# Optimization experiments

Hardware: AMD Instinct MI355X
Metric: run time of the kernel (lower is better)

## Reference

```python
import jax, jax.numpy as jnp
import numpy as np

N_SEG = 65536          # number of output segments
TOTAL = 2097152        # total input rows (avg 32 per segment)
D = 128                # feature dim


def setup_inputs() -> dict:
    key = jax.random.key(0)
    kx, kp = jax.random.split(key)
    x = jax.random.normal(kx, (TOTAL, D), dtype=jnp.float32)
    # CSR indptr: sorted random interior boundaries, endpoints pinned to 0 and TOTAL
    inner = jnp.sort(jax.random.randint(kp, (N_SEG - 1,), 0, TOTAL, dtype=jnp.int64))
    indptr = jnp.concatenate([
        jnp.zeros((1,), dtype=jnp.int64),
        inner,
        jnp.full((1,), TOTAL, dtype=jnp.int64),
    ])  # [N_SEG + 1]
    return {"x": x, "indptr": indptr}


def _indptr_to_segment_ids(indptr, total):
    # Marker-and-cumsum: handles empty segments (duplicate indptr values) via .add
    marks = jnp.zeros((total,), dtype=jnp.int32)
    marks = marks.at[indptr[1:-1]].add(1)
    return jnp.cumsum(marks)  # [total] segment id per row


def reference(x, indptr):
    # segment_csr(x, indptr, reduce='sum'): out[i] = sum of x[indptr[i]:indptr[i+1]]
    seg_ids = _indptr_to_segment_ids(indptr, x.shape[0])
    return jax.ops.segment_sum(x, seg_ids, num_segments=N_SEG)  # [N_SEG, D]
```

## Files before the change

### kernel.cpp

```cpp
#include <hip/hip_runtime.h>


#define NSEG  65536
#define TOTAL 2097152
#define RPW   128
#define UNR   8

typedef float f32x2 __attribute__((ext_vector_type(2)));
typedef float f32x4 __attribute__((ext_vector_type(4)));

__global__ __launch_bounds__(256) void zero_out_kernel(f32x4* __restrict__ out4)
{
    const size_t i = (size_t)blockIdx.x * 256 + threadIdx.x;
    f32x4 z = {0.f, 0.f, 0.f, 0.f};
    __builtin_nontemporal_store(z, out4 + i);
}

__global__ __launch_bounds__(256) void segcsr_sweep(
    const f32x2* __restrict__ x,
    const int*   __restrict__ indptr,
    float*       __restrict__ out)
{
    const int wid  = __builtin_amdgcn_readfirstlane((blockIdx.x << 2) + (threadIdx.x >> 6));
    const int lane = threadIdx.x & 63;
    const int r0 = wid * RPW;
    const int r1 = r0 + RPW;

    int lo = 0, hi = NSEG;
    while (hi - lo > 1) {
        const int mid = (lo + hi) >> 1;
        if (indptr[mid] <= r0) lo = mid; else hi = mid;
    }
    int s        = lo;
    int segBegin = indptr[s];
    int segEnd   = indptr[s + 1];

    float ax = 0.f, ay = 0.f;
    int lastFlush = r0;

    for (int base = r0; base < r1; base += UNR) {
        f32x2 v[UNR];
#pragma unroll
        for (int j = 0; j < UNR; ++j)
            v[j] = __builtin_nontemporal_load(&x[(size_t)(base + j) * 64 + lane]);
#pragma unroll
        for (int j = 0; j < UNR; ++j) {
            ax += v[j].x;
            ay += v[j].y;
            const int rr = base + j + 1;
            if (rr == segEnd) {
                float* o = out + (size_t)s * 128 + lane * 2;
                if (segBegin >= r0) {
                    o[0] = ax; o[1] = ay;
                } else {
                    atomicAdd(o,     ax);
                    atomicAdd(o + 1, ay);
                }
                ax = 0.f; ay = 0.f;
                lastFlush = rr;
                if (rr < TOTAL) {
                    do { s++; } while (indptr[s + 1] <= rr);
                    segBegin = rr;
                    segEnd   = indptr[s + 1];
                }
            }
        }
    }

    if (lastFlush < r1) {
        float* o = out + (size_t)s * 128 + lane * 2;
        atomicAdd(o,     ax);
        atomicAdd(o + 1, ay);
    }
}

extern "C" void kernel_launch(void* const* d_in, const int* in_sizes, int n_in,
                              void* d_out, int out_size, void* d_ws, size_t ws_size,
                              hipStream_t stream) {
    const f32x2* x      = (const f32x2*)d_in[0];
    const int*   indptr = (const int*)d_in[1];
    float*       out    = (float*)d_out;

    zero_out_kernel<<<dim3(8192), dim3(256), 0, stream>>>((f32x4*)out);

    segcsr_sweep<<<dim3(TOTAL / RPW / 4), dim3(256), 0, stream>>>(x, indptr, out);
}
```

Baseline: 1.372 ms.

## Process two rows per wave with float4 loads and cross-half shuffle reduction

```diff
diff --git a/kernel.cpp b/kernel.cpp
--- a/kernel.cpp
+++ b/kernel.cpp
@@ -3,10 +3,9 @@
 
 #define NSEG  65536
 #define TOTAL 2097152
-#define RPW   128
-#define UNR   8
+#define RPW   256
+#define UNRP  8
 
-typedef float f32x2 __attribute__((ext_vector_type(2)));
 typedef float f32x4 __attribute__((ext_vector_type(4)));
 
 __global__ __launch_bounds__(256) void zero_out_kernel(f32x4* __restrict__ out4)
@@ -17,67 +16,97 @@
 }
 
 __global__ __launch_bounds__(256) void segcsr_sweep(
-    const f32x2* __restrict__ x,
+    const f32x4* __restrict__ x,
     const int*   __restrict__ indptr,
     float*       __restrict__ out)
 {
     const int wid  = __builtin_amdgcn_readfirstlane((blockIdx.x << 2) + (threadIdx.x >> 6));
     const int lane = threadIdx.x & 63;
-    const int r0 = wid * RPW;
-    const int r1 = r0 + RPW;
+    const int c    = lane & 31;
+    const int rh   = lane >> 5;
+    const int r0   = wid * RPW;
+    const int r1   = r0 + RPW;
 
     int lo = 0, hi = NSEG;
     while (hi - lo > 1) {
         const int mid = (lo + hi) >> 1;
         if (indptr[mid] <= r0) lo = mid; else hi = mid;
     }
-    int s        = lo;
-    int segBegin = indptr[s];
-    int segEnd   = indptr[s + 1];
-
-    float ax = 0.f, ay = 0.f;
+    int s         = lo;
+    int segBegin  = indptr[s];
+    int segEnd    = indptr[s + 1];
     int lastFlush = r0;
 
-    for (int base = r0; base < r1; base += UNR) {
-        f32x2 v[UNR];
+    f32x4 acc = {0.f, 0.f, 0.f, 0.f};
+
+    auto FLUSH = [&](int rr) {
+        float tx = acc.x + __shfl_down(acc.x, 32);
+        float ty = acc.y + __shfl_down(acc.y, 32);
+        float tz = acc.z + __shfl_down(acc.z, 32);
+        float tw = acc.w + __shfl_down(acc.w, 32);
+        if (rh == 0) {
+            float* o = out + (size_t)s * 128 + c * 4;
+            if (segBegin >= r0) {
+                f32x4 t = {tx, ty, tz, tw};
+                __builtin_nontemporal_store(t, (f32x4*)o);
+            } else {
+                atomicAdd(o,     tx);
+                atomicAdd(o + 1, ty);
+                atomicAdd(o + 2, tz);
+                atomicAdd(o + 3, tw);
+            }
+        }
+        acc.x = 0.f; acc.y = 0.f; acc.z = 0.f; acc.w = 0.f;
+        lastFlush = rr;
+        if (rr < r1) {
+            do { s++; } while (indptr[s + 1] <= rr);
+            segBegin = rr;
+            segEnd   = indptr[s + 1];
+        }
+    };
+
+    for (int base = r0; base < r1; base += 2 * UNRP) {
+        f32x4 v[UNRP];
 #pragma unroll
-        for (int j = 0; j < UNR; ++j)
-            v[j] = __builtin_nontemporal_load(&x[(size_t)(base + j) * 64 + lane]);
+        for (int j = 0; j < UNRP; ++j)
+            v[j] = __builtin_nontemporal_load(&x[(size_t)(base + 2 * j + rh) * 32 + c]);
 #pragma unroll
-        for (int j = 0; j < UNR; ++j) {
-            ax += v[j].x;
-            ay += v[j].y;
-            const int rr = base + j + 1;
-            if (rr == segEnd) {
-                float* o = out + (size_t)s * 128 + lane * 2;
-                if (segBegin >= r0) {
-                    o[0] = ax; o[1] = ay;
-                } else {
-                    atomicAdd(o,     ax);
-                    atomicAdd(o + 1, ay);
-                }
-                ax = 0.f; ay = 0.f;
-                lastFlush = rr;
-                if (rr < TOTAL) {
-                    do { s++; } while (indptr[s + 1] <= rr);
-                    segBegin = rr;
-                    segEnd   = indptr[s + 1];
-                }
+        for (int j = 0; j < UNRP; ++j) {
+            const int b   = base + 2 * j;
+            const int rr1 = b + 1;
+            const int rr2 = b + 2;
+            if (segEnd == rr1) {
+                if (rh == 0) acc += v[j];
+                FLUSH(rr1);
+                if (rh == 1) acc += v[j];
+            } else {
+                acc += v[j];
+            }
+            if (segEnd == rr2) {
+                FLUSH(rr2);
             }
         }
     }
 
     if (lastFlush < r1) {
-        float* o = out + (size_t)s * 128 + lane * 2;
-        atomicAdd(o,     ax);
-        atomicAdd(o + 1, ay);
+        float tx = acc.x + __shfl_down(acc.x, 32);
+        float ty = acc.y + __shfl_down(acc.y, 32);
+        float tz = acc.z + __shfl_down(acc.z, 32);
+        float tw = acc.w + __shfl_down(acc.w, 32);
+        if (rh == 0) {
+            float* o = out + (size_t)s * 128 + c * 4;
+            atomicAdd(o,     tx);
+            atomicAdd(o + 1, ty);
+            atomicAdd(o + 2, tz);
+            atomicAdd(o + 3, tw);
+        }
     }
 }
 
 extern "C" void kernel_launch(void* const* d_in, const int* in_sizes, int n_in,
                               void* d_out, int out_size, void* d_ws, size_t ws_size,
                               hipStream_t stream) {
-    const f32x2* x      = (const f32x2*)d_in[0];
+    const f32x4* x      = (const f32x4*)d_in[0];
     const int*   indptr = (const int*)d_in[1];
     float*       out    = (float*)d_out;
 
```

After: 1.330 ms. 3.1% less time.
